# Kernel tuning notes

Hardware: AMD Instinct MI355X
Metric: run time of the kernel (lower is better)

Reference implementation:

```python
import jax, jax.numpy as jnp
import numpy as np

EPS = 1e-8
COMMITMENT_COST = 0.25
NUM_EMBEDDINGS = 8192
EMBEDDING_DIM = 256


def setup_inputs() -> dict:
    key = jax.random.key(0)
    k1, k2 = jax.random.split(key)
    z = jax.random.normal(k1, (4, 4096, EMBEDDING_DIM), dtype=jnp.float32)
    # nn.Embedding init: uniform(-1/K, 1/K)
    lim = 1.0 / NUM_EMBEDDINGS
    codebook = jax.random.uniform(k2, (NUM_EMBEDDINGS, EMBEDDING_DIM), dtype=jnp.float32,
                                  minval=-lim, maxval=lim)
    return {"z": z, "codebook": codebook}


def reference(z, codebook):
    input_shape = z.shape
    flat = z.reshape(-1, EMBEDDING_DIM)              # [N, D]
    # squared euclidean distances (argmin identical to cdist argmin)
    d2 = (jnp.sum(flat * flat, axis=1, keepdims=True)
          - 2.0 * flat @ codebook.T
          + jnp.sum(codebook * codebook, axis=1))    # [N, K]
    indices = jnp.argmin(d2, axis=1)                 # [N]
    c_star = codebook[indices]                       # [N, D] gather
    d_vec = c_star - flat
    # eval mode: v_d = d_vec (no noise)
    magnitude = jnp.linalg.norm(d_vec, axis=1, keepdims=True)          # [N, 1]
    direction = jax.lax.stop_gradient(
        d_vec / (jnp.linalg.norm(d_vec, axis=1, keepdims=True) + EPS))  # [N, D]
    z_q = (flat + magnitude * direction).reshape(input_shape)
    codebook_loss = jnp.mean((c_star - jax.lax.stop_gradient(flat)) ** 2)
    commitment_loss = jnp.mean((flat - jax.lax.stop_gradient(c_star)) ** 2)
    loss = codebook_loss + COMMITMENT_COST * commitment_loss
    return z_q, loss, indices.reshape(input_shape[:-1])
```

## Files before the change

### kernel.cpp

```cpp
#include <hip/hip_runtime.h>
#include <math.h>

#define NROWS 16384
#define KC 8192
#define DD 256
#define CAP 128
#define MARGIN 3.0e-4f

typedef __attribute__((ext_vector_type(8))) short bf16x8;
typedef __attribute__((ext_vector_type(4))) float f32x4;

__device__ __forceinline__ unsigned short f2bf(float f) {
    unsigned int u = __float_as_uint(f);
    unsigned int r = (u + 0x7FFFu + ((u >> 16) & 1u)) >> 16;
    return (unsigned short)r;
}
__device__ __forceinline__ unsigned int fenc(float f) {
    unsigned int u = __float_as_uint(f);
    return (u & 0x80000000u) ? ~u : (u | 0x80000000u);
}
__device__ __forceinline__ float fdec(unsigned int u) {
    return __uint_as_float((u & 0x80000000u) ? (u & 0x7FFFFFFFu) : ~u);
}

__device__ __forceinline__ float exact_d2(const float* __restrict__ zrow,
                                          const float* __restrict__ crow,
                                          float A, float C)
{
    float dot = 0.0f;
#pragma unroll 8
    for (int d = 0; d < 64; ++d) {
        const float4 zv = *(const float4*)(zrow + 4 * d);
        const float4 cv = *(const float4*)(crow + 4 * d);
        dot = fmaf(zv.x, cv.x, dot);
        dot = fmaf(zv.y, cv.y, dot);
        dot = fmaf(zv.z, cv.z, dot);
        dot = fmaf(zv.w, cv.w, dot);
    }
    return __fadd_rn(__fsub_rn(A, 2.0f * dot), C);
}

__global__ __launch_bounds__(256)
void vq_prep(const float* __restrict__ z, const float* __restrict__ cb,
             unsigned short* __restrict__ zb, unsigned short* __restrict__ cbb,
             float* __restrict__ cc, float* __restrict__ rowA,
             int* __restrict__ cnt, unsigned int* __restrict__ rmin,
             float* __restrict__ loss_ptr)
{
    const int t = threadIdx.x;
    const int b = blockIdx.x;
    const size_t i = (size_t)b * 256 + t;
    {
        const float* src; unsigned short* dst; size_t off;
        if (i < 1048576) { src = z;  dst = zb;  off = i; }
        else             { src = cb; dst = cbb; off = i - 1048576; }
        float4 v = *(const float4*)(src + off * 4);
        ushort4 o;
        o.x = f2bf(v.x); o.y = f2bf(v.y); o.z = f2bf(v.z); o.w = f2bf(v.w);
        *(ushort4*)(dst + off * 4) = o;
    }
    if (b < 1536) {
        const int unit = b * 16 + (t >> 4);
        const int l = t & 15;
        const float* p = (unit < KC) ? (cb + (size_t)unit * DD)
                                     : (z + (size_t)(unit - KC) * DD);
        const float* q = p + 128 * (l >> 3) + (l & 7);
        float x0 = q[0];
        float r = __fmul_rn(x0, x0);
#pragma unroll
        for (int k = 1; k < 16; ++k) {
            const float x = q[8 * k];
            r = __fadd_rn(r, __fmul_rn(x, x));
        }
        r = __fadd_rn(r, __shfl_xor(r, 1, 64));
        r = __fadd_rn(r, __shfl_xor(r, 2, 64));
        r = __fadd_rn(r, __shfl_xor(r, 4, 64));
        r = __fadd_rn(r, __shfl_xor(r, 8, 64));
        if (l == 0) {
            if (unit < KC) cc[unit] = r;
            else rowA[unit - KC] = r;
        }
    } else if (b < 1664) {
        const int u = (b - 1536) * 256 + t;
        if (u < NROWS) cnt[u] = 0;
        else rmin[u - NROWS] = 0xFFFFFFFFu;
    }
    if (i == 0) *loss_ptr = 0.0f;
}

__global__ __launch_bounds__(512, 2)
void vq_gemm_screen(const unsigned short* __restrict__ cbb,
                    const unsigned short* __restrict__ zb,
                    const float* __restrict__ cc,
                    unsigned int* __restrict__ rowmin_u,
                    int* __restrict__ cnt, int* __restrict__ cand)
{
    __shared__ char Als[2][32768];
    __shared__ char Bls[2][32768];
    __shared__ float ccs[256];
    __shared__ float colmin_lds[4][256];
    __shared__ float thr_lds[256];

    const int t = threadIdx.x;
    const int lane = t & 63;
    const int w = t >> 6;
    const int cw = w >> 1;
    const int rw = w & 1;
    const int gr = blockIdx.x;
    const int gc = blockIdx.y;

    const char* gA = (const char*)(cbb + (size_t)gc * 256 * DD);
    const char* gB = (const char*)(zb  + (size_t)gr * 256 * DD);

    if (t < 256) ccs[t] = cc[gc * 256 + t];

    f32x4 acc[4][8];
#pragma unroll
    for (int i = 0; i < 4; ++i)
#pragma unroll
        for (int j = 0; j < 8; ++j) acc[i][j] = (f32x4)0.0f;

    const int rA = lane & 15;
    const int kq = (lane >> 4) * 16;

    auto STAGE = [&](int bsel, int kc) {
#pragma unroll
        for (int i = 0; i < 4; ++i) {
            const int o = (w * 4 + i) * 1024 + lane * 16;
            const int row = o >> 7;
            const int col = (o & 127) ^ ((row & 7) << 4);
            const int gofs = row * 512 + kc * 128 + col;
            __builtin_amdgcn_global_load_lds(
                (const unsigned int*)(gA + gofs),
                (unsigned int*)(Als[bsel] + (w * 4 + i) * 1024), 16, 0, 0);
            __builtin_amdgcn_global_load_lds(
                (const unsigned int*)(gB + gofs),
                (unsigned int*)(Bls[bsel] + (w * 4 + i) * 1024), 16, 0, 0);
        }
    };

    STAGE(0, 0);
    int cur = 0;
    for (int kc = 0; kc < 4; ++kc) {
        __syncthreads();
        if (kc < 3) STAGE(cur ^ 1, kc + 1);
#pragma unroll
        for (int ks = 0; ks < 2; ++ks) {
            bf16x8 af[4], bfr[8];
#pragma unroll
            for (int i = 0; i < 4; ++i) {
                const int c = cw * 64 + i * 16 + rA;
                af[i] = *(const bf16x8*)(Als[cur] + c * 128 +
                         ((ks * 64 + kq) ^ ((c & 7) << 4)));
            }
#pragma unroll
            for (int j = 0; j < 8; ++j) {
                const int r = rw * 128 + j * 16 + rA;
                bfr[j] = *(const bf16x8*)(Bls[cur] + r * 128 +
                          ((ks * 64 + kq) ^ ((r & 7) << 4)));
            }
#pragma unroll
            for (int i = 0; i < 4; ++i)
#pragma unroll
                for (int j = 0; j < 8; ++j)
                    acc[i][j] = __builtin_amdgcn_mfma_f32_16x16x32_bf16(
                        af[i], bfr[j], acc[i][j], 0, 0, 0);
        }
        cur ^= 1;
    }

    const int lr = lane >> 4;
    float mj[8];
#pragma unroll
    for (int j = 0; j < 8; ++j) mj[j] = 3.0e38f;
#pragma unroll
    for (int i = 0; i < 4; ++i) {
#pragma unroll
        for (int r = 0; r < 4; ++r) {
            const float ccv = ccs[cw * 64 + i * 16 + lr * 4 + r];
#pragma unroll
            for (int j = 0; j < 8; ++j) {
                const float d = fmaf(-2.0f, acc[i][j][r], ccv);
                acc[i][j][r] = d;
                mj[j] = fminf(mj[j], d);
            }
        }
    }
#pragma unroll
    for (int j = 0; j < 8; ++j) {
        mj[j] = fminf(mj[j], __shfl_xor(mj[j], 16, 64));
        mj[j] = fminf(mj[j], __shfl_xor(mj[j], 32, 64));
        colmin_lds[cw][rw * 128 + j * 16 + rA] = mj[j];
    }
    __syncthreads();

    if (t < 256) {
        const float cm = fminf(fminf(colmin_lds[0][t], colmin_lds[1][t]),
                               fminf(colmin_lds[2][t], colmin_lds[3][t]));
        const unsigned int enc = fenc(cm);
        const unsigned int old = atomicMin(&rowmin_u[gr * 256 + t], enc);
        const unsigned int curm = (old < enc) ? old : enc;
        thr_lds[t] = fdec(curm) + MARGIN;
    }
    __syncthreads();

#pragma unroll
    for (int j = 0; j < 8; ++j) {
        const int colL = rw * 128 + j * 16 + rA;
        const float thr = thr_lds[colL];
        const int rowg = gr * 256 + colL;
#pragma unroll
        for (int i = 0; i < 4; ++i)
#pragma unroll
            for (int r = 0; r < 4; ++r)
                if (acc[i][j][r] <= thr) {
                    const int pos = atomicAdd(&cnt[rowg], 1);
                    if (pos < CAP)
                        cand[(size_t)rowg * CAP + pos] =
                            gc * 256 + cw * 64 + i * 16 + lr * 4 + r;
                }
    }
}

__global__ __launch_bounds__(256)
void vq_finalize_out(const float* __restrict__ z, const float* __restrict__ cb,
                     const float* __restrict__ rowA, const float* __restrict__ cc,
                     const int* __restrict__ cnt, const int* __restrict__ cand,
                     float* __restrict__ zq, float* __restrict__ loss_ptr,
                     float* __restrict__ idx_out)
{
    __shared__ float wsum[4];
    const int t = threadIdx.x;
    const int lane = t & 63;
    const int w = t >> 6;
    const int row = blockIdx.x * 4 + w;
    const int n = cnt[row];
    const float A = rowA[row];
    const float* zrow = z + (size_t)row * DD;

    int bidx = 0x7FFFFFFF;
    bool need_full = (n < 1 || n > CAP);
    if (!need_full) {
        if (n == 1) {
            bidx = cand[(size_t)row * CAP];
            if ((unsigned)bidx >= (unsigned)KC) need_full = true;
        } else {
            float best = 3.0e38f;
            for (int base = 0; base < n; base += 64) {
                const int ci = base + lane;
                float d2 = 3.0e38f;
                int code = 0x7FFFFFFF;
                if (ci < n) {
                    code = cand[(size_t)row * CAP + ci];
                    if ((unsigned)code < (unsigned)KC)
                        d2 = exact_d2(zrow, cb + (size_t)code * DD, A, cc[code]);
                    else
                        code = 0x7FFFFFFF;
                }
                if (d2 < best || (d2 == best && code < bidx)) { best = d2; bidx = code; }
            }
#pragma unroll
            for (int m = 1; m < 64; m <<= 1) {
                const float ov = __shfl_xor(best, m, 64);
                const int oi = __shfl_xor(bidx, m, 64);
                if (ov < best || (ov == best && oi < bidx)) { best = ov; bidx = oi; }
            }
            if ((unsigned)bidx >= (unsigned)KC) need_full = true;
        }
    }
    if (need_full) {
        float best = 3.0e38f;
        bidx = 0x7FFFFFFF;
        for (int code = lane; code < KC; code += 64) {
            const float d2 = exact_d2(zrow, cb + (size_t)code * DD, A, cc[code]);
            if (d2 < best || (d2 == best && code < bidx)) { best = d2; bidx = code; }
        }
#pragma unroll
        for (int m = 1; m < 64; m <<= 1) {
            const float ov = __shfl_xor(best, m, 64);
            const int oi = __shfl_xor(bidx, m, 64);
            if (ov < best || (ov == best && oi < bidx)) { best = ov; bidx = oi; }
        }
        if ((unsigned)bidx >= (unsigned)KC) bidx = 0;
    }

    const int k = bidx;
    const float4 z4 = *(const float4*)(zrow + lane * 4);
    const float4 c4 = *(const float4*)(cb + (size_t)k * DD + lane * 4);
    float4 d4 = make_float4(c4.x - z4.x, c4.y - z4.y, c4.z - z4.z, c4.w - z4.w);
    float ss = fmaf(d4.x, d4.x, fmaf(d4.y, d4.y, fmaf(d4.z, d4.z, d4.w * d4.w)));
#pragma unroll
    for (int m = 1; m < 64; m <<= 1) ss += __shfl_xor(ss, m, 64);
    const float mag = sqrtf(ss);
    const float scale = mag / (mag + 1e-8f);
    float4 q = make_float4(fmaf(scale, d4.x, z4.x), fmaf(scale, d4.y, z4.y),
                           fmaf(scale, d4.z, z4.z), fmaf(scale, d4.w, z4.w));
    *(float4*)(zq + (size_t)row * DD + lane * 4) = q;
    if (lane == 0) {
        wsum[w] = ss;
        idx_out[row] = (float)k;
    }
    __syncthreads();
    if (t == 0) {
        const float s = (wsum[0] + wsum[1]) + (wsum[2] + wsum[3]);
        atomicAdd(loss_ptr, s * (1.25f / 4194304.0f));
    }
}

extern "C" void kernel_launch(void* const* d_in, const int* in_sizes, int n_in,
                              void* d_out, int out_size, void* d_ws, size_t ws_size,
                              hipStream_t stream)
{
    (void)in_sizes; (void)n_in; (void)out_size; (void)ws_size;
    const float* z = (const float*)d_in[0];
    const float* cb = (const float*)d_in[1];
    float* out = (float*)d_out;
    float* zq = out;
    float* loss_ptr = out + (size_t)NROWS * DD;
    float* idx_out = loss_ptr + 1;

    char* ws = (char*)d_ws;
    unsigned short* zb   = (unsigned short*)(ws);
    unsigned short* cbb  = (unsigned short*)(ws + 8388608);
    int*            cand = (int*)(ws + 12582912);
    int*            cnt  = (int*)(ws + 20971520);
    unsigned int*   rmin = (unsigned int*)(ws + 21037056);
    float*          cc   = (float*)(ws + 21102592);
    float*          rowA = (float*)(ws + 21135360);

    vq_prep<<<6144, 256, 0, stream>>>(z, cb, zb, cbb, cc, rowA, cnt, rmin, loss_ptr);
    vq_gemm_screen<<<dim3(NROWS / 256, KC / 256), 512, 0, stream>>>(
        cbb, zb, cc, rmin, cnt, cand);
    vq_finalize_out<<<NROWS / 4, 256, 0, stream>>>(
        z, cb, rowA, cc, cnt, cand, zq, loss_ptr, idx_out);
}
```

Measured before the change: 275.2 us.

## Keep z rows in registers and stream whole codebook per block

The GEMM screen is restructured so each block owns 64 z rows held in registers and loops over all 32 codebook tiles, streaming codebook chunks through double-buffered LDS. The running row minimum moves from a global atomicMin into shared memory, so thresholds tighten progressively within a block and fewer candidates are emitted. This trades 2048 large blocks for 256 long-running blocks with a smaller per-wave tile (4x2 MFMAs). That lowers arithmetic intensity per LDS load and adds two barriers per codebook tile.

```diff
diff --git a/kernel.cpp b/kernel.cpp
--- a/kernel.cpp
+++ b/kernel.cpp
@@ -10,17 +10,16 @@
 typedef __attribute__((ext_vector_type(8))) short bf16x8;
 typedef __attribute__((ext_vector_type(4))) float f32x4;
 
+#define LGKM_BAR() do { \
+    asm volatile("s_waitcnt lgkmcnt(0)" ::: "memory"); \
+    __builtin_amdgcn_sched_barrier(0); \
+    __builtin_amdgcn_s_barrier(); \
+    __builtin_amdgcn_sched_barrier(0); } while (0)
+
 __device__ __forceinline__ unsigned short f2bf(float f) {
     unsigned int u = __float_as_uint(f);
     unsigned int r = (u + 0x7FFFu + ((u >> 16) & 1u)) >> 16;
     return (unsigned short)r;
-}
-__device__ __forceinline__ unsigned int fenc(float f) {
-    unsigned int u = __float_as_uint(f);
-    return (u & 0x80000000u) ? ~u : (u | 0x80000000u);
-}
-__device__ __forceinline__ float fdec(unsigned int u) {
-    return __uint_as_float((u & 0x80000000u) ? (u & 0x7FFFFFFFu) : ~u);
 }
 
 __device__ __forceinline__ float exact_d2(const float* __restrict__ zrow,
@@ -92,133 +91,128 @@
 void vq_gemm_screen(const unsigned short* __restrict__ cbb,
                     const unsigned short* __restrict__ zb,
                     const float* __restrict__ cc,
-                    unsigned int* __restrict__ rowmin_u,
                     int* __restrict__ cnt, int* __restrict__ cand)
 {
     __shared__ char Als[2][32768];
-    __shared__ char Bls[2][32768];
     __shared__ float ccs[256];
-    __shared__ float colmin_lds[4][256];
-    __shared__ float thr_lds[256];
+    __shared__ float colmin[4][64];
+    __shared__ float rowminS[64];
+    __shared__ float thr_lds[64];
 
     const int t = threadIdx.x;
     const int lane = t & 63;
     const int w = t >> 6;
     const int cw = w >> 1;
     const int rw = w & 1;
-    const int gr = blockIdx.x;
-    const int gc = blockIdx.y;
-
-    const char* gA = (const char*)(cbb + (size_t)gc * 256 * DD);
-    const char* gB = (const char*)(zb  + (size_t)gr * 256 * DD);
-
-    if (t < 256) ccs[t] = cc[gc * 256 + t];
-
-    f32x4 acc[4][8];
-#pragma unroll
-    for (int i = 0; i < 4; ++i)
-#pragma unroll
-        for (int j = 0; j < 8; ++j) acc[i][j] = (f32x4)0.0f;
-
+    const int rowbase = blockIdx.x * 64;
     const int rA = lane & 15;
-    const int kq = (lane >> 4) * 16;
-
-    auto STAGE = [&](int bsel, int kc) {
+    const int lr = lane >> 4;
+    const int kq = lr * 16;
+
+    if (t < 64) rowminS[t] = 3.0e38f;
+
+    bf16x8 zreg[2][8];
+#pragma unroll
+    for (int j = 0; j < 2; ++j) {
+        const int row = rowbase + rw * 32 + j * 16 + rA;
+        const unsigned short* zr = zb + (size_t)row * DD + lr * 8;
+#pragma unroll
+        for (int kg = 0; kg < 8; ++kg)
+            zreg[j][kg] = *(const bf16x8*)(zr + kg * 32);
+    }
+
+    auto STAGE = [&](int b, int c) {
+        const char* gA = (const char*)cbb + (size_t)(c >> 2) * 256 * 512;
+        const int kc = c & 3;
 #pragma unroll
         for (int i = 0; i < 4; ++i) {
-            const int o = (w * 4 + i) * 1024 + lane * 16;
+            const int o = i * 8192 + w * 1024 + lane * 16;
             const int row = o >> 7;
             const int col = (o & 127) ^ ((row & 7) << 4);
-            const int gofs = row * 512 + kc * 128 + col;
             __builtin_amdgcn_global_load_lds(
-                (const unsigned int*)(gA + gofs),
-                (unsigned int*)(Als[bsel] + (w * 4 + i) * 1024), 16, 0, 0);
-            __builtin_amdgcn_global_load_lds(
-                (const unsigned int*)(gB + gofs),
-                (unsigned int*)(Bls[bsel] + (w * 4 + i) * 1024), 16, 0, 0);
+                (const unsigned int*)(gA + row * 512 + kc * 128 + col),
+                (unsigned int*)(Als[b] + i * 8192 + w * 1024), 16, 0, 0);
         }
     };
 
     STAGE(0, 0);
     int cur = 0;
-    for (int kc = 0; kc < 4; ++kc) {
-        __syncthreads();
-        if (kc < 3) STAGE(cur ^ 1, kc + 1);
-#pragma unroll
-        for (int ks = 0; ks < 2; ++ks) {
-            bf16x8 af[4], bfr[8];
-#pragma unroll
-            for (int i = 0; i < 4; ++i) {
-                const int c = cw * 64 + i * 16 + rA;
-                af[i] = *(const bf16x8*)(Als[cur] + c * 128 +
-                         ((ks * 64 + kq) ^ ((c & 7) << 4)));
+    for (int gc = 0; gc < 32; ++gc) {
+        f32x4 acc[4][2];
+#pragma unroll
+        for (int i = 0; i < 4; ++i)
+#pragma unroll
+            for (int j = 0; j < 2; ++j) acc[i][j] = (f32x4)0.0f;
+
+#pragma unroll
+        for (int kc = 0; kc < 4; ++kc) {
+            __syncthreads();
+            if (kc == 0 && t < 256) ccs[t] = cc[gc * 256 + t];
+            const int cnext = gc * 4 + kc + 1;
+            if (cnext < 128) STAGE(cur ^ 1, cnext);
+#pragma unroll
+            for (int ks = 0; ks < 2; ++ks) {
+                bf16x8 af[4];
+#pragma unroll
+                for (int i = 0; i < 4; ++i) {
+                    const int c = cw * 64 + i * 16 + rA;
+                    af[i] = *(const bf16x8*)(Als[cur] + c * 128 +
+                             ((ks * 64 + kq) ^ ((c & 7) << 4)));
+                }
+#pragma unroll
+                for (int i = 0; i < 4; ++i)
+#pragma unroll
+                    for (int j = 0; j < 2; ++j)
+                        acc[i][j] = __builtin_amdgcn_mfma_f32_16x16x32_bf16(
+                            af[i], zreg[j][kc * 2 + ks], acc[i][j], 0, 0, 0);
             }
-#pragma unroll
-            for (int j = 0; j < 8; ++j) {
-                const int r = rw * 128 + j * 16 + rA;
-                bfr[j] = *(const bf16x8*)(Bls[cur] + r * 128 +
-                          ((ks * 64 + kq) ^ ((r & 7) << 4)));
+            cur ^= 1;
+        }
+
+        float mj[2] = {3.0e38f, 3.0e38f};
+#pragma unroll
+        for (int i = 0; i < 4; ++i)
+#pragma unroll
+            for (int r = 0; r < 4; ++r) {
+                const float ccv = ccs[cw * 64 + i * 16 + lr * 4 + r];
+#pragma unroll
+                for (int j = 0; j < 2; ++j) {
+                    const float d = fmaf(-2.0f, acc[i][j][r], ccv);
+                    acc[i][j][r] = d;
+                    mj[j] = fminf(mj[j], d);
+                }
             }
 #pragma unroll
+        for (int j = 0; j < 2; ++j) {
+            mj[j] = fminf(mj[j], __shfl_xor(mj[j], 16, 64));
+            mj[j] = fminf(mj[j], __shfl_xor(mj[j], 32, 64));
+            if (lr == 0) colmin[cw][rw * 32 + j * 16 + rA] = mj[j];
+        }
+        LGKM_BAR();
+        if (t < 64) {
+            const float cm = fminf(fminf(colmin[0][t], colmin[1][t]),
+                                   fminf(colmin[2][t], colmin[3][t]));
+            const float rm = fminf(rowminS[t], cm);
+            rowminS[t] = rm;
+            thr_lds[t] = rm + MARGIN;
+        }
+        LGKM_BAR();
+#pragma unroll
+        for (int j = 0; j < 2; ++j) {
+            const int rloc = rw * 32 + j * 16 + rA;
+            const float thr = thr_lds[rloc];
+            const int rowg = rowbase + rloc;
+#pragma unroll
             for (int i = 0; i < 4; ++i)
 #pragma unroll
-                for (int j = 0; j < 8; ++j)
-                    acc[i][j] = __builtin_amdgcn_mfma_f32_16x16x32_bf16(
-                        af[i], bfr[j], acc[i][j], 0, 0, 0);
-        }
-        cur ^= 1;
-    }
-
-    const int lr = lane >> 4;
-    float mj[8];
-#pragma unroll
-    for (int j = 0; j < 8; ++j) mj[j] = 3.0e38f;
-#pragma unroll
-    for (int i = 0; i < 4; ++i) {
-#pragma unroll
-        for (int r = 0; r < 4; ++r) {
-            const float ccv = ccs[cw * 64 + i * 16 + lr * 4 + r];
-#pragma unroll
-            for (int j = 0; j < 8; ++j) {
-                const float d = fmaf(-2.0f, acc[i][j][r], ccv);
-                acc[i][j][r] = d;
-                mj[j] = fminf(mj[j], d);
-            }
-        }
-    }
-#pragma unroll
-    for (int j = 0; j < 8; ++j) {
-        mj[j] = fminf(mj[j], __shfl_xor(mj[j], 16, 64));
-        mj[j] = fminf(mj[j], __shfl_xor(mj[j], 32, 64));
-        colmin_lds[cw][rw * 128 + j * 16 + rA] = mj[j];
-    }
-    __syncthreads();
-
-    if (t < 256) {
-        const float cm = fminf(fminf(colmin_lds[0][t], colmin_lds[1][t]),
-                               fminf(colmin_lds[2][t], colmin_lds[3][t]));
-        const unsigned int enc = fenc(cm);
-        const unsigned int old = atomicMin(&rowmin_u[gr * 256 + t], enc);
-        const unsigned int curm = (old < enc) ? old : enc;
-        thr_lds[t] = fdec(curm) + MARGIN;
-    }
-    __syncthreads();
-
-#pragma unroll
-    for (int j = 0; j < 8; ++j) {
-        const int colL = rw * 128 + j * 16 + rA;
-        const float thr = thr_lds[colL];
-        const int rowg = gr * 256 + colL;
-#pragma unroll
-        for (int i = 0; i < 4; ++i)
-#pragma unroll
-            for (int r = 0; r < 4; ++r)
-                if (acc[i][j][r] <= thr) {
-                    const int pos = atomicAdd(&cnt[rowg], 1);
-                    if (pos < CAP)
-                        cand[(size_t)rowg * CAP + pos] =
-                            gc * 256 + cw * 64 + i * 16 + lr * 4 + r;
-                }
+                for (int r = 0; r < 4; ++r)
+                    if (acc[i][j][r] <= thr) {
+                        const int pos = atomicAdd(&cnt[rowg], 1);
+                        if (pos < CAP)
+                            cand[(size_t)rowg * CAP + pos] =
+                                gc * 256 + cw * 64 + i * 16 + lr * 4 + r;
+                    }
+        }
     }
 }
 
@@ -329,8 +323,7 @@
     float*          rowA = (float*)(ws + 21135360);
 
     vq_prep<<<6144, 256, 0, stream>>>(z, cb, zb, cbb, cc, rowA, cnt, rmin, loss_ptr);
-    vq_gemm_screen<<<dim3(NROWS / 256, KC / 256), 512, 0, stream>>>(
-        cbb, zb, cc, rmin, cnt, cand);
+    vq_gemm_screen<<<NROWS / 64, 512, 0, stream>>>(cbb, zb, cc, cnt, cand);
     vq_finalize_out<<<NROWS / 4, 256, 0, stream>>>(
         z, cb, rowA, cc, cnt, cand, zq, loss_ptr, idx_out);
 }
```

Measured after the change: 305.4 us. +11.0%, slower.
